# Optimization experiments

Hardware: AMD Instinct MI355X
Metric: run time of the kernel (lower is better)

## Reference

```python
import jax, jax.numpy as jnp
import numpy as np


def setup_inputs() -> dict:
    key = jax.random.key(0)
    kq, kk = jax.random.split(key)
    B, H, T, D = 4, 12, 2048, 64
    q = jax.random.normal(kq, (B, H, T, D), dtype=jnp.float32)
    k = jax.random.normal(kk, (B, H, T, D), dtype=jnp.float32)
    return {"q": q, "k": k, "T": T, "block_size": T}


def reference(q, k, T, block_size):
    # scaled QK^T: [B,H,T,T]
    scale = k.shape[-1] ** (-0.5)
    scores = jnp.einsum("bhqd,bhkd->bhqk", q, k) * scale
    # causal mask (tril[:T,:T] == 0 -> -inf); T == seq len here
    causal = jnp.tril(jnp.ones((T, T), dtype=bool))
    scores = jnp.where(causal, scores, -jnp.inf)
    # softmax over keys; dropout=0.0 (eval / p=0) is identity
    return jax.nn.softmax(scores, axis=-1)
```

## Files before the change

kernel.cpp:

```cpp
#include <hip/hip_runtime.h>

#define T_DIM 2048
#define D_DIM 64
#define BH 48

typedef _Float16 f16x8 __attribute__((ext_vector_type(8)));
typedef _Float16 f16x4 __attribute__((ext_vector_type(4)));
typedef float f32x4 __attribute__((ext_vector_type(4)));

__global__ void cvt_f32_f16(const float* __restrict__ src, _Float16* __restrict__ dst, int n4) {
    int i = blockIdx.x * blockDim.x + threadIdx.x;
    if (i >= n4) return;
    float4 v = ((const float4* __restrict__)src)[i];
    f16x4 h = { (_Float16)v.x, (_Float16)v.y, (_Float16)v.z, (_Float16)v.w };
    ((f16x4*)dst)[i] = h;
}

__global__ __launch_bounds__(256) void sdp_kernel(const _Float16* __restrict__ q16,
                                                  const _Float16* __restrict__ k16,
                                                  float* __restrict__ out) {
    const int T = T_DIM;
    const float scale = 0.125f;

    int bh   = blockIdx.x >> 4;
    int qblk = blockIdx.x & 15;
    int wave = threadIdx.x >> 6;
    int lane = threadIdx.x & 63;
    int g    = lane >> 4;
    int li   = lane & 15;
    int qbase = qblk * 128 + wave * 32;

    const _Float16* qh = q16 + (size_t)bh * T * D_DIM;
    const _Float16* kh = k16 + (size_t)bh * T * D_DIM;
    float* oh = out + (size_t)bh * T * T;

    f16x8 a_lo[2], a_hi[2];
#pragma unroll
    for (int mt = 0; mt < 2; ++mt) {
        const _Float16* p = qh + (size_t)(qbase + mt * 16 + li) * D_DIM;
        a_lo[mt] = *(const f16x8*)(p + g * 8);
        a_hi[mt] = *(const f16x8*)(p + 32 + g * 8);
    }

    int ktmax = (qbase + 31) >> 4;

    float sum[2][4] = {{0.f,0.f,0.f,0.f},{0.f,0.f,0.f,0.f}};
    for (int kt = 0; kt <= ktmax; ++kt) {
        int c = kt * 16 + li;
        const _Float16* p = kh + (size_t)c * D_DIM;
        f16x8 b_lo = *(const f16x8*)(p + g * 8);
        f16x8 b_hi = *(const f16x8*)(p + 32 + g * 8);
#pragma unroll
        for (int mt = 0; mt < 2; ++mt) {
            f32x4 acc = {0.f, 0.f, 0.f, 0.f};
            acc = __builtin_amdgcn_mfma_f32_16x16x32_f16(a_lo[mt], b_lo, acc, 0, 0, 0);
            acc = __builtin_amdgcn_mfma_f32_16x16x32_f16(a_hi[mt], b_hi, acc, 0, 0, 0);
#pragma unroll
            for (int reg = 0; reg < 4; ++reg) {
                int r = qbase + mt * 16 + g * 4 + reg;
                float e = (c <= r) ? __expf(acc[reg] * scale) : 0.f;
                sum[mt][reg] += e;
            }
        }
    }

    float rinv[2][4];
#pragma unroll
    for (int mt = 0; mt < 2; ++mt)
#pragma unroll
        for (int reg = 0; reg < 4; ++reg) {
            float s = sum[mt][reg];
            s += __shfl_xor(s, 1);
            s += __shfl_xor(s, 2);
            s += __shfl_xor(s, 4);
            s += __shfl_xor(s, 8);
            rinv[mt][reg] = 1.0f / s;
        }

    for (int kt = 0; kt <= ktmax; ++kt) {
        int c = kt * 16 + li;
        const _Float16* p = kh + (size_t)c * D_DIM;
        f16x8 b_lo = *(const f16x8*)(p + g * 8);
        f16x8 b_hi = *(const f16x8*)(p + 32 + g * 8);
#pragma unroll
        for (int mt = 0; mt < 2; ++mt) {
            f32x4 acc = {0.f, 0.f, 0.f, 0.f};
            acc = __builtin_amdgcn_mfma_f32_16x16x32_f16(a_lo[mt], b_lo, acc, 0, 0, 0);
            acc = __builtin_amdgcn_mfma_f32_16x16x32_f16(a_hi[mt], b_hi, acc, 0, 0, 0);
#pragma unroll
            for (int reg = 0; reg < 4; ++reg) {
                int r = qbase + mt * 16 + g * 4 + reg;
                float pv = (c <= r) ? __expf(acc[reg] * scale) * rinv[mt][reg] : 0.f;
                oh[(size_t)r * T + c] = pv;
            }
        }
    }

    int zstart = (ktmax + 1) * 16;
    float4 z = make_float4(0.f, 0.f, 0.f, 0.f);
    for (int rr = 0; rr < 32; ++rr) {
        float* rowp = oh + (size_t)(qbase + rr) * T;
        for (int cc = zstart + lane * 4; cc < T; cc += 256)
            *(float4*)(rowp + cc) = z;
    }
}

extern "C" void kernel_launch(void* const* d_in, const int* in_sizes, int n_in,
                              void* d_out, int out_size, void* d_ws, size_t ws_size,
                              hipStream_t stream) {
    const float* q = (const float*)d_in[0];
    const float* k = (const float*)d_in[1];
    float* out = (float*)d_out;

    _Float16* q16 = (_Float16*)d_ws;
    _Float16* k16 = q16 + (size_t)BH * T_DIM * D_DIM;

    int n  = BH * T_DIM * D_DIM;
    int n4 = n / 4;
    cvt_f32_f16<<<(n4 + 255) / 256, 256, 0, stream>>>(q, q16, n4);
    cvt_f32_f16<<<(n4 + 255) / 256, 256, 0, stream>>>(k, k16, n4);

    sdp_kernel<<<BH * 16, 256, 0, stream>>>(q16, k16, out);
}
```

Baseline: 1.008 ms.

## Swap MFMA operands so each lane writes contiguous float4 output rows

The MFMA operands are swapped (K as A, Q as B), which transposes the accumulator layout so each lane holds four consecutive key columns of one query row. The output can then be written with 16-byte vector stores instead of scattered scalar stores. The causal mask is now applied only on the two diagonal tiles, so the off-diagonal loops skip per-element comparisons. Row sums are reduced with two shuffles instead of four per register. The cost is more specialised, unrolled code for the diagonal tiles.

```diff
diff --git a/kernel.cpp b/kernel.cpp
--- a/kernel.cpp
+++ b/kernel.cpp
@@ -34,69 +34,121 @@
     const _Float16* kh = k16 + (size_t)bh * T * D_DIM;
     float* oh = out + (size_t)bh * T * T;
 
-    f16x8 a_lo[2], a_hi[2];
+    f16x8 b_lo[2], b_hi[2];
 #pragma unroll
     for (int mt = 0; mt < 2; ++mt) {
         const _Float16* p = qh + (size_t)(qbase + mt * 16 + li) * D_DIM;
-        a_lo[mt] = *(const f16x8*)(p + g * 8);
-        a_hi[mt] = *(const f16x8*)(p + 32 + g * 8);
+        b_lo[mt] = *(const f16x8*)(p + g * 8);
+        b_hi[mt] = *(const f16x8*)(p + 32 + g * 8);
     }
 
-    int ktmax = (qbase + 31) >> 4;
+    const int kb = qbase >> 4;
 
-    float sum[2][4] = {{0.f,0.f,0.f,0.f},{0.f,0.f,0.f,0.f}};
-    for (int kt = 0; kt <= ktmax; ++kt) {
-        int c = kt * 16 + li;
-        const _Float16* p = kh + (size_t)c * D_DIM;
-        f16x8 b_lo = *(const f16x8*)(p + g * 8);
-        f16x8 b_hi = *(const f16x8*)(p + 32 + g * 8);
+    float sum0 = 0.f, sum1 = 0.f;
+    for (int kt = 0; kt < kb; ++kt) {
+        const _Float16* p = kh + (size_t)(kt * 16 + li) * D_DIM;
+        f16x8 a_lo = *(const f16x8*)(p + g * 8);
+        f16x8 a_hi = *(const f16x8*)(p + 32 + g * 8);
+        f32x4 acc0 = {0.f, 0.f, 0.f, 0.f}, acc1 = {0.f, 0.f, 0.f, 0.f};
+        acc0 = __builtin_amdgcn_mfma_f32_16x16x32_f16(a_lo, b_lo[0], acc0, 0, 0, 0);
+        acc0 = __builtin_amdgcn_mfma_f32_16x16x32_f16(a_hi, b_hi[0], acc0, 0, 0, 0);
+        acc1 = __builtin_amdgcn_mfma_f32_16x16x32_f16(a_lo, b_lo[1], acc1, 0, 0, 0);
+        acc1 = __builtin_amdgcn_mfma_f32_16x16x32_f16(a_hi, b_hi[1], acc1, 0, 0, 0);
 #pragma unroll
-        for (int mt = 0; mt < 2; ++mt) {
-            f32x4 acc = {0.f, 0.f, 0.f, 0.f};
-            acc = __builtin_amdgcn_mfma_f32_16x16x32_f16(a_lo[mt], b_lo, acc, 0, 0, 0);
-            acc = __builtin_amdgcn_mfma_f32_16x16x32_f16(a_hi[mt], b_hi, acc, 0, 0, 0);
-#pragma unroll
-            for (int reg = 0; reg < 4; ++reg) {
-                int r = qbase + mt * 16 + g * 4 + reg;
-                float e = (c <= r) ? __expf(acc[reg] * scale) : 0.f;
-                sum[mt][reg] += e;
-            }
+        for (int e = 0; e < 4; ++e) {
+            sum0 += __expf(acc0[e] * scale);
+            sum1 += __expf(acc1[e] * scale);
         }
     }
-
-    float rinv[2][4];
+    {
+        const _Float16* p = kh + (size_t)(kb * 16 + li) * D_DIM;
+        f16x8 a_lo = *(const f16x8*)(p + g * 8);
+        f16x8 a_hi = *(const f16x8*)(p + 32 + g * 8);
+        f32x4 acc0 = {0.f, 0.f, 0.f, 0.f}, acc1 = {0.f, 0.f, 0.f, 0.f};
+        acc0 = __builtin_amdgcn_mfma_f32_16x16x32_f16(a_lo, b_lo[0], acc0, 0, 0, 0);
+        acc0 = __builtin_amdgcn_mfma_f32_16x16x32_f16(a_hi, b_hi[0], acc0, 0, 0, 0);
+        acc1 = __builtin_amdgcn_mfma_f32_16x16x32_f16(a_lo, b_lo[1], acc1, 0, 0, 0);
+        acc1 = __builtin_amdgcn_mfma_f32_16x16x32_f16(a_hi, b_hi[1], acc1, 0, 0, 0);
+        int d = li - g * 4;
 #pragma unroll
-    for (int mt = 0; mt < 2; ++mt)
-#pragma unroll
-        for (int reg = 0; reg < 4; ++reg) {
-            float s = sum[mt][reg];
-            s += __shfl_xor(s, 1);
-            s += __shfl_xor(s, 2);
-            s += __shfl_xor(s, 4);
-            s += __shfl_xor(s, 8);
-            rinv[mt][reg] = 1.0f / s;
-        }
-
-    for (int kt = 0; kt <= ktmax; ++kt) {
-        int c = kt * 16 + li;
-        const _Float16* p = kh + (size_t)c * D_DIM;
-        f16x8 b_lo = *(const f16x8*)(p + g * 8);
-        f16x8 b_hi = *(const f16x8*)(p + 32 + g * 8);
-#pragma unroll
-        for (int mt = 0; mt < 2; ++mt) {
-            f32x4 acc = {0.f, 0.f, 0.f, 0.f};
-            acc = __builtin_amdgcn_mfma_f32_16x16x32_f16(a_lo[mt], b_lo, acc, 0, 0, 0);
-            acc = __builtin_amdgcn_mfma_f32_16x16x32_f16(a_hi[mt], b_hi, acc, 0, 0, 0);
-#pragma unroll
-            for (int reg = 0; reg < 4; ++reg) {
-                int r = qbase + mt * 16 + g * 4 + reg;
-                float pv = (c <= r) ? __expf(acc[reg] * scale) * rinv[mt][reg] : 0.f;
-                oh[(size_t)r * T + c] = pv;
-            }
+        for (int e = 0; e < 4; ++e) {
+            sum0 += (e <= d) ? __expf(acc0[e] * scale) : 0.f;
+            sum1 += __expf(acc1[e] * scale);
         }
     }
+    {
+        const _Float16* p = kh + (size_t)((kb + 1) * 16 + li) * D_DIM;
+        f16x8 a_lo = *(const f16x8*)(p + g * 8);
+        f16x8 a_hi = *(const f16x8*)(p + 32 + g * 8);
+        f32x4 acc1 = {0.f, 0.f, 0.f, 0.f};
+        acc1 = __builtin_amdgcn_mfma_f32_16x16x32_f16(a_lo, b_lo[1], acc1, 0, 0, 0);
+        acc1 = __builtin_amdgcn_mfma_f32_16x16x32_f16(a_hi, b_hi[1], acc1, 0, 0, 0);
+        int d = li - g * 4;
+#pragma unroll
+        for (int e = 0; e < 4; ++e)
+            sum1 += (e <= d) ? __expf(acc1[e] * scale) : 0.f;
+    }
+    sum0 += __shfl_xor(sum0, 16); sum0 += __shfl_xor(sum0, 32);
+    sum1 += __shfl_xor(sum1, 16); sum1 += __shfl_xor(sum1, 32);
+    float rinv0 = 1.0f / sum0;
+    float rinv1 = 1.0f / sum1;
 
-    int zstart = (ktmax + 1) * 16;
+    float* rp0 = oh + (size_t)(qbase + li) * T + g * 4;
+    float* rp1 = rp0 + (size_t)16 * T;
+    for (int kt = 0; kt < kb; ++kt) {
+        const _Float16* p = kh + (size_t)(kt * 16 + li) * D_DIM;
+        f16x8 a_lo = *(const f16x8*)(p + g * 8);
+        f16x8 a_hi = *(const f16x8*)(p + 32 + g * 8);
+        f32x4 acc0 = {0.f, 0.f, 0.f, 0.f}, acc1 = {0.f, 0.f, 0.f, 0.f};
+        acc0 = __builtin_amdgcn_mfma_f32_16x16x32_f16(a_lo, b_lo[0], acc0, 0, 0, 0);
+        acc0 = __builtin_amdgcn_mfma_f32_16x16x32_f16(a_hi, b_hi[0], acc0, 0, 0, 0);
+        acc1 = __builtin_amdgcn_mfma_f32_16x16x32_f16(a_lo, b_lo[1], acc1, 0, 0, 0);
+        acc1 = __builtin_amdgcn_mfma_f32_16x16x32_f16(a_hi, b_hi[1], acc1, 0, 0, 0);
+        f32x4 pv0, pv1;
+#pragma unroll
+        for (int e = 0; e < 4; ++e) {
+            pv0[e] = __expf(acc0[e] * scale) * rinv0;
+            pv1[e] = __expf(acc1[e] * scale) * rinv1;
+        }
+        *(f32x4*)(rp0 + kt * 16) = pv0;
+        *(f32x4*)(rp1 + kt * 16) = pv1;
+    }
+    {
+        const _Float16* p = kh + (size_t)(kb * 16 + li) * D_DIM;
+        f16x8 a_lo = *(const f16x8*)(p + g * 8);
+        f16x8 a_hi = *(const f16x8*)(p + 32 + g * 8);
+        f32x4 acc0 = {0.f, 0.f, 0.f, 0.f}, acc1 = {0.f, 0.f, 0.f, 0.f};
+        acc0 = __builtin_amdgcn_mfma_f32_16x16x32_f16(a_lo, b_lo[0], acc0, 0, 0, 0);
+        acc0 = __builtin_amdgcn_mfma_f32_16x16x32_f16(a_hi, b_hi[0], acc0, 0, 0, 0);
+        acc1 = __builtin_amdgcn_mfma_f32_16x16x32_f16(a_lo, b_lo[1], acc1, 0, 0, 0);
+        acc1 = __builtin_amdgcn_mfma_f32_16x16x32_f16(a_hi, b_hi[1], acc1, 0, 0, 0);
+        int d = li - g * 4;
+        f32x4 pv0, pv1;
+#pragma unroll
+        for (int e = 0; e < 4; ++e) {
+            pv0[e] = (e <= d) ? __expf(acc0[e] * scale) * rinv0 : 0.f;
+            pv1[e] = __expf(acc1[e] * scale) * rinv1;
+        }
+        *(f32x4*)(rp0 + kb * 16) = pv0;
+        *(f32x4*)(rp1 + kb * 16) = pv1;
+    }
+    {
+        const _Float16* p = kh + (size_t)((kb + 1) * 16 + li) * D_DIM;
+        f16x8 a_lo = *(const f16x8*)(p + g * 8);
+        f16x8 a_hi = *(const f16x8*)(p + 32 + g * 8);
+        f32x4 acc1 = {0.f, 0.f, 0.f, 0.f};
+        acc1 = __builtin_amdgcn_mfma_f32_16x16x32_f16(a_lo, b_lo[1], acc1, 0, 0, 0);
+        acc1 = __builtin_amdgcn_mfma_f32_16x16x32_f16(a_hi, b_hi[1], acc1, 0, 0, 0);
+        int d = li - g * 4;
+        f32x4 pv1, z4 = {0.f, 0.f, 0.f, 0.f};
+#pragma unroll
+        for (int e = 0; e < 4; ++e)
+            pv1[e] = (e <= d) ? __expf(acc1[e] * scale) * rinv1 : 0.f;
+        *(f32x4*)(rp0 + (kb + 1) * 16) = z4;
+        *(f32x4*)(rp1 + (kb + 1) * 16) = pv1;
+    }
+
+    int zstart = qbase + 32;
     float4 z = make_float4(0.f, 0.f, 0.f, 0.f);
     for (int rr = 0; rr < 32; ++rr) {
         float* rowp = oh + (size_t)(qbase + rr) * T;
```

After: 1.017 ms. Within noise of the previous version (+0.9%).
